# Performance work log

Measured on AMD Instinct MI355X. Metric: run time of the kernel, lower is better.

## Reference

```python
import jax, jax.numpy as jnp
import numpy as np
import math

B, M, N = 1, 128, 256
LIG_C = 256      # rep_1d num_c
ATTN_C = 32      # attention_num_c
HEADS = 8        # num_heads
EPS = 1e-5


def setup_inputs() -> dict:
    key = jax.random.key(0)
    ks = jax.random.split(key, 8)
    s = 1.0 / math.sqrt(LIG_C)
    return {
        "lig_profile": jax.random.normal(ks[0], (B, M, N, LIG_C), dtype=jnp.float32),
        "ln_scale": jnp.ones((LIG_C,), dtype=jnp.float32),
        "ln_bias": jnp.zeros((LIG_C,), dtype=jnp.float32),
        "wq": jax.random.normal(ks[1], (LIG_C, ATTN_C * HEADS), dtype=jnp.float32) * s,
        "wk": jax.random.normal(ks[2], (LIG_C, ATTN_C * HEADS), dtype=jnp.float32) * s,
        "wv": jax.random.normal(ks[3], (LIG_C, ATTN_C * HEADS), dtype=jnp.float32) * s,
        "wf": jax.random.normal(ks[4], (ATTN_C * HEADS, LIG_C), dtype=jnp.float32) * s,
        "bf": jnp.zeros((LIG_C,), dtype=jnp.float32),
    }


def reference(lig_profile, ln_scale, ln_bias, wq, wk, wv, wf, bf):
    # LayerNorm over channel dim
    mu = jnp.mean(lig_profile, axis=-1, keepdims=True)
    var = jnp.mean(jnp.square(lig_profile - mu), axis=-1, keepdims=True)
    x = (lig_profile - mu) * jax.lax.rsqrt(var + EPS) * ln_scale + ln_bias

    # QKV projections; view splits last dim as (attn_c, heads) -> channel-major layout
    shape5 = x.shape[:-1] + (ATTN_C, HEADS)
    q = (x @ wq).reshape(shape5)  # [b,m,n,c,h]
    k = (x @ wk).reshape(shape5)
    v = (x @ wv).reshape(shape5)

    factor = 1.0 / math.sqrt(ATTN_C)
    aff = jnp.einsum('bmich,bmjch->bmijh', q, k) * factor  # [b,m,i,j,h]
    weights = jax.nn.softmax(aff, axis=-2)                  # softmax over j (keys)
    out = jnp.einsum('bmrch,bmirh->bmich', v, weights)      # [b,m,i,c,h]
    out = out.reshape(out.shape[:-2] + (ATTN_C * HEADS,))
    return out @ wf + bf
```

## Files before the change

### kernel.cpp

```cpp
#include <hip/hip_runtime.h>

typedef _Float16 f16;
typedef _Float16 f16x8 __attribute__((ext_vector_type(8)));
typedef _Float16 f16x4 __attribute__((ext_vector_type(4)));
typedef float f32x4 __attribute__((ext_vector_type(4)));

#define MDIM 128
#define NDIM 256
#define CDIM 256
#define ROWS (MDIM*NDIM)

__global__ __launch_bounds__(256) void k_prep(
    const float* __restrict__ wq, const float* __restrict__ wk,
    const float* __restrict__ wv, const float* __restrict__ wf,
    f16* __restrict__ bq, f16* __restrict__ bk, f16* __restrict__ bv,
    f16* __restrict__ bw)
{
  int idx   = blockIdx.x & 255;
  int which = blockIdx.x >> 8;
  int kk    = threadIdx.x;
  if (which < 3) {
    const float* W = which == 0 ? wq : which == 1 ? wk : wv;
    f16* dst       = which == 0 ? bq : which == 1 ? bk : bv;
    float sc = which == 0 ? 0.17677669529663689f : 1.0f;
    int j = (idx & 31) * 8 + (idx >> 5);
    dst[idx * 256 + kk] = (f16)(W[(size_t)kk * 256 + j] * sc);
  } else {
    int pk = (kk & 31) * 8 + (kk >> 5);
    bw[idx * 256 + kk] = (f16)wf[(size_t)pk * 256 + idx];
  }
}

__global__ __launch_bounds__(256) void k_ln(const float* __restrict__ x,
                                            const float* __restrict__ g,
                                            const float* __restrict__ b,
                                            f16* __restrict__ y)
{
  int row  = blockIdx.x * 4 + (threadIdx.x >> 6);
  int lane = threadIdx.x & 63;
  const float4 xv = *(const float4*)(x + (size_t)row * CDIM + lane * 4);
  float s  = xv.x + xv.y + xv.z + xv.w;
  float s2 = xv.x*xv.x + xv.y*xv.y + xv.z*xv.z + xv.w*xv.w;
#pragma unroll
  for (int m = 1; m < 64; m <<= 1) {
    s  += __shfl_xor(s,  m, 64);
    s2 += __shfl_xor(s2, m, 64);
  }
  float mu  = s * (1.0f / CDIM);
  float var = s2 * (1.0f / CDIM) - mu * mu;
  float rs  = rsqrtf(var + 1e-5f);
  const float4 gv = *(const float4*)(g + lane * 4);
  const float4 bv = *(const float4*)(b + lane * 4);
  f16x4 o;
  o[0] = (f16)((xv.x - mu) * rs * gv.x + bv.x);
  o[1] = (f16)((xv.y - mu) * rs * gv.y + bv.y);
  o[2] = (f16)((xv.z - mu) * rs * gv.z + bv.z);
  o[3] = (f16)((xv.w - mu) * rs * gv.w + bv.w);
  *(f16x4*)(y + (size_t)row * CDIM + lane * 4) = o;
}

__global__ __launch_bounds__(256) void k_qkv(const f16* __restrict__ x,
    const f16* __restrict__ bq, const f16* __restrict__ bk, const f16* __restrict__ bv,
    f16* __restrict__ q, f16* __restrict__ k, f16* __restrict__ v)
{
  __shared__ f16 As[64][264];
  __shared__ f16 Bs[64][264];
  int bm = blockIdx.x;
  int t = threadIdx.x, lane = t & 63, w = t >> 6;
  int wr = w >> 1, wc = w & 1;
  int l15 = lane & 15, l4 = lane >> 4;
#pragma unroll
  for (int p = 0; p < 8; ++p) {
    int r = t >> 2, c0 = (t & 3) * 8 + p * 32;
    *(f16x8*)&As[r][c0] = *(const f16x8*)(x + (size_t)(bm * 64 + r) * 256 + c0);
  }
  for (int ct = 0; ct < 12; ++ct) {
    const f16* B = ct < 4 ? bq : ct < 8 ? bk : bv;
    f16* dst     = ct < 4 ? q  : ct < 8 ? k  : v;
    int je0 = (ct & 3) * 64;
#pragma unroll
    for (int p = 0; p < 8; ++p) {
      int r = t >> 2, c0 = (t & 3) * 8 + p * 32;
      *(f16x8*)&Bs[r][c0] = *(const f16x8*)(B + (size_t)(je0 + r) * 256 + c0);
    }
    __syncthreads();
    f32x4 acc[2][2] = {};
#pragma unroll
    for (int kt = 0; kt < 8; ++kt) {
      f16x8 a0 = *(const f16x8*)&As[wr * 32 +      l15][kt * 32 + l4 * 8];
      f16x8 a1 = *(const f16x8*)&As[wr * 32 + 16 + l15][kt * 32 + l4 * 8];
      f16x8 b0 = *(const f16x8*)&Bs[wc * 32 +      l15][kt * 32 + l4 * 8];
      f16x8 b1 = *(const f16x8*)&Bs[wc * 32 + 16 + l15][kt * 32 + l4 * 8];
      acc[0][0] = __builtin_amdgcn_mfma_f32_16x16x32_f16(a0, b0, acc[0][0], 0, 0, 0);
      acc[0][1] = __builtin_amdgcn_mfma_f32_16x16x32_f16(a0, b1, acc[0][1], 0, 0, 0);
      acc[1][0] = __builtin_amdgcn_mfma_f32_16x16x32_f16(a1, b0, acc[1][0], 0, 0, 0);
      acc[1][1] = __builtin_amdgcn_mfma_f32_16x16x32_f16(a1, b1, acc[1][1], 0, 0, 0);
    }
#pragma unroll
    for (int mi = 0; mi < 2; ++mi)
#pragma unroll
      for (int ni = 0; ni < 2; ++ni)
#pragma unroll
        for (int r = 0; r < 4; ++r) {
          int row = bm * 64 + wr * 32 + mi * 16 + l4 * 4 + r;
          int col = je0 + wc * 32 + ni * 16 + l15;
          dst[(size_t)row * 256 + col] = (f16)acc[mi][ni][r];
        }
    __syncthreads();
  }
}

__global__ __launch_bounds__(256) void k_attn(const f16* __restrict__ q,
    const f16* __restrict__ k, const f16* __restrict__ v, f16* __restrict__ o)
{
  __shared__ f16 ks[256][40];
  __shared__ f16 vt[32][264];
  __shared__ f16 ps[4][16][264];
  int m = blockIdx.x >> 3, h = blockIdx.x & 7;
  int t = threadIdx.x, lane = t & 63, w = t >> 6;
  int l15 = lane & 15, l4 = lane >> 4;
  size_t base = ((size_t)m * 256) * 256 + h * 32;
#pragma unroll
  for (int p = 0; p < 4; ++p) {
    int n = p * 64 + (t >> 2);
    int c0 = (t & 3) * 8;
    *(f16x8*)&ks[n][c0] = *(const f16x8*)(k + base + (size_t)n * 256 + c0);
    f16x8 vv = *(const f16x8*)(v + base + (size_t)n * 256 + c0);
#pragma unroll
    for (int i = 0; i < 8; ++i) vt[c0 + i][n] = vv[i];
  }
  __syncthreads();
  for (int ch = 0; ch < 4; ++ch) {
    int i0 = w * 64 + ch * 16;
    f16x8 qa = *(const f16x8*)(q + base + (size_t)(i0 + l15) * 256 + l4 * 8);
    f32x4 s[16];
#pragma unroll
    for (int jf = 0; jf < 16; ++jf) {
      f16x8 kb = *(const f16x8*)&ks[jf * 16 + l15][l4 * 8];
      f32x4 z = {0.f, 0.f, 0.f, 0.f};
      s[jf] = __builtin_amdgcn_mfma_f32_16x16x32_f16(qa, kb, z, 0, 0, 0);
    }
#pragma unroll
    for (int r = 0; r < 4; ++r) {
      float mx = s[0][r];
#pragma unroll
      for (int jf = 1; jf < 16; ++jf) mx = fmaxf(mx, s[jf][r]);
      mx = fmaxf(mx, __shfl_xor(mx, 1, 64));
      mx = fmaxf(mx, __shfl_xor(mx, 2, 64));
      mx = fmaxf(mx, __shfl_xor(mx, 4, 64));
      mx = fmaxf(mx, __shfl_xor(mx, 8, 64));
      float sum = 0.f;
#pragma unroll
      for (int jf = 0; jf < 16; ++jf) {
        float e = __expf(s[jf][r] - mx);
        s[jf][r] = e;
        sum += e;
      }
      sum += __shfl_xor(sum, 1, 64);
      sum += __shfl_xor(sum, 2, 64);
      sum += __shfl_xor(sum, 4, 64);
      sum += __shfl_xor(sum, 8, 64);
      float inv = 1.f / sum;
#pragma unroll
      for (int jf = 0; jf < 16; ++jf)
        ps[w][l4 * 4 + r][jf * 16 + l15] = (f16)(s[jf][r] * inv);
    }
    f32x4 o0 = {0.f,0.f,0.f,0.f}, o1 = {0.f,0.f,0.f,0.f};
#pragma unroll
    for (int kk = 0; kk < 8; ++kk) {
      f16x8 pa  = *(const f16x8*)&ps[w][l15][kk * 32 + l4 * 8];
      f16x8 vb0 = *(const f16x8*)&vt[l15][kk * 32 + l4 * 8];
      f16x8 vb1 = *(const f16x8*)&vt[16 + l15][kk * 32 + l4 * 8];
      o0 = __builtin_amdgcn_mfma_f32_16x16x32_f16(pa, vb0, o0, 0, 0, 0);
      o1 = __builtin_amdgcn_mfma_f32_16x16x32_f16(pa, vb1, o1, 0, 0, 0);
    }
#pragma unroll
    for (int r = 0; r < 4; ++r) {
      size_t ro = base + (size_t)(i0 + l4 * 4 + r) * 256;
      o[ro + l15]      = (f16)o0[r];
      o[ro + 16 + l15] = (f16)o1[r];
    }
  }
}

__global__ __launch_bounds__(256) void k_out(const f16* __restrict__ a,
    const f16* __restrict__ bw, const float* __restrict__ bias,
    float* __restrict__ out)
{
  __shared__ f16 As[64][264];
  __shared__ f16 Bs[64][264];
  int bm = blockIdx.x;
  int t = threadIdx.x, lane = t & 63, w = t >> 6;
  int wr = w >> 1, wc = w & 1;
  int l15 = lane & 15, l4 = lane >> 4;
#pragma unroll
  for (int p = 0; p < 8; ++p) {
    int r = t >> 2, c0 = (t & 3) * 8 + p * 32;
    *(f16x8*)&As[r][c0] = *(const f16x8*)(a + (size_t)(bm * 64 + r) * 256 + c0);
  }
  for (int ct = 0; ct < 4; ++ct) {
    int col0 = ct * 64;
#pragma unroll
    for (int p = 0; p < 8; ++p) {
      int r = t >> 2, c0 = (t & 3) * 8 + p * 32;
      *(f16x8*)&Bs[r][c0] = *(const f16x8*)(bw + (size_t)(col0 + r) * 256 + c0);
    }
    __syncthreads();
    f32x4 acc[2][2] = {};
#pragma unroll
    for (int kt = 0; kt < 8; ++kt) {
      f16x8 a0 = *(const f16x8*)&As[wr * 32 +      l15][kt * 32 + l4 * 8];
      f16x8 a1 = *(const f16x8*)&As[wr * 32 + 16 + l15][kt * 32 + l4 * 8];
      f16x8 b0 = *(const f16x8*)&Bs[wc * 32 +      l15][kt * 32 + l4 * 8];
      f16x8 b1 = *(const f16x8*)&Bs[wc * 32 + 16 + l15][kt * 32 + l4 * 8];
      acc[0][0] = __builtin_amdgcn_mfma_f32_16x16x32_f16(a0, b0, acc[0][0], 0, 0, 0);
      acc[0][1] = __builtin_amdgcn_mfma_f32_16x16x32_f16(a0, b1, acc[0][1], 0, 0, 0);
      acc[1][0] = __builtin_amdgcn_mfma_f32_16x16x32_f16(a1, b0, acc[1][0], 0, 0, 0);
      acc[1][1] = __builtin_amdgcn_mfma_f32_16x16x32_f16(a1, b1, acc[1][1], 0, 0, 0);
    }
#pragma unroll
    for (int mi = 0; mi < 2; ++mi)
#pragma unroll
      for (int ni = 0; ni < 2; ++ni)
#pragma unroll
        for (int r = 0; r < 4; ++r) {
          int row = bm * 64 + wr * 32 + mi * 16 + l4 * 4 + r;
          int col = col0 + wc * 32 + ni * 16 + l15;
          out[(size_t)row * 256 + col] = acc[mi][ni][r] + bias[col];
        }
    __syncthreads();
  }
}

extern "C" void kernel_launch(void* const* d_in, const int* in_sizes, int n_in,
                              void* d_out, int out_size, void* d_ws, size_t ws_size,
                              hipStream_t stream)
{
  const float* x  = (const float*)d_in[0];
  const float* g  = (const float*)d_in[1];
  const float* b  = (const float*)d_in[2];
  const float* wq = (const float*)d_in[3];
  const float* wk = (const float*)d_in[4];
  const float* wv = (const float*)d_in[5];
  const float* wf = (const float*)d_in[6];
  const float* bf = (const float*)d_in[7];
  float* out = (float*)d_out;

  char* ws = (char*)d_ws;
  f16* xh = (f16*)(ws);
  f16* qh = (f16*)(ws + (size_t)16 * 1024 * 1024);
  f16* kh = (f16*)(ws + (size_t)32 * 1024 * 1024);
  f16* vh = (f16*)(ws + (size_t)48 * 1024 * 1024);
  char* wbase = ws + (size_t)64 * 1024 * 1024;
  f16* bq = (f16*)(wbase);
  f16* bk = (f16*)(wbase + 128 * 1024);
  f16* bv = (f16*)(wbase + 256 * 1024);
  f16* bw = (f16*)(wbase + 384 * 1024);

  k_prep<<<1024,      256, 0, stream>>>(wq, wk, wv, wf, bq, bk, bv, bw);
  k_ln  <<<ROWS / 4,  256, 0, stream>>>(x, g, b, xh);
  k_qkv <<<ROWS / 64, 256, 0, stream>>>(xh, bq, bk, bv, qh, kh, vh);
  k_attn<<<MDIM * 8,  256, 0, stream>>>(qh, kh, vh, xh);
  k_out <<<ROWS / 64, 256, 0, stream>>>(xh, bw, bf, out);
}
```

Measured before the change: 98.34 us.

## Fuse LayerNorm into QKV GEMM, emit transposed V, use flash-style 32x32 attention

LayerNorm is fused into the QKV projection kernel, which removes one launch and the fp16 activation round trip through memory. The QKV kernel now writes V pre-transposed through an LDS staging tile, so the attention kernel loads it with vectorized reads instead of scalar transposed stores. Attention is rewritten as an online-softmax loop using 32x32x16 MFMAs, exp2 with log2(e) folded into the Q weights, and a lazy rescale that skips rescaling when the running max changes little. Probabilities are passed between lanes with shuffles instead of LDS, and the grid is split into query halves to give more blocks. The cost is more shuffle traffic and more complex register-level data movement.

Result: faster. 84.05 us (-14.5%).

```diff
diff --git a/kernel.cpp b/kernel.cpp
--- a/kernel.cpp
+++ b/kernel.cpp
@@ -3,12 +3,20 @@
 typedef _Float16 f16;
 typedef _Float16 f16x8 __attribute__((ext_vector_type(8)));
 typedef _Float16 f16x4 __attribute__((ext_vector_type(4)));
+typedef _Float16 f16x2 __attribute__((ext_vector_type(2)));
 typedef float f32x4 __attribute__((ext_vector_type(4)));
+typedef float f32x16 __attribute__((ext_vector_type(16)));
 
 #define MDIM 128
 #define NDIM 256
 #define CDIM 256
 #define ROWS (MDIM*NDIM)
+
+__device__ inline int pk2(float a, float b) {
+  union { f16x2 h; int i; } u;
+  u.h[0] = (f16)a; u.h[1] = (f16)b;
+  return u.i;
+}
 
 __global__ __launch_bounds__(256) void k_prep(
     const float* __restrict__ wq, const float* __restrict__ wk,
@@ -22,61 +30,52 @@
   if (which < 3) {
     const float* W = which == 0 ? wq : which == 1 ? wk : wv;
     f16* dst       = which == 0 ? bq : which == 1 ? bk : bv;
-    float sc = which == 0 ? 0.17677669529663689f : 1.0f;
+    float sc = which == 0 ? (0.17677669529663689f * 1.4426950408889634f) : 1.0f;
     int j = (idx & 31) * 8 + (idx >> 5);
     dst[idx * 256 + kk] = (f16)(W[(size_t)kk * 256 + j] * sc);
   } else {
-    int pk = (kk & 31) * 8 + (kk >> 5);
-    bw[idx * 256 + kk] = (f16)wf[(size_t)pk * 256 + idx];
-  }
-}
-
-__global__ __launch_bounds__(256) void k_ln(const float* __restrict__ x,
-                                            const float* __restrict__ g,
-                                            const float* __restrict__ b,
-                                            f16* __restrict__ y)
-{
-  int row  = blockIdx.x * 4 + (threadIdx.x >> 6);
-  int lane = threadIdx.x & 63;
-  const float4 xv = *(const float4*)(x + (size_t)row * CDIM + lane * 4);
-  float s  = xv.x + xv.y + xv.z + xv.w;
-  float s2 = xv.x*xv.x + xv.y*xv.y + xv.z*xv.z + xv.w*xv.w;
-#pragma unroll
-  for (int m = 1; m < 64; m <<= 1) {
-    s  += __shfl_xor(s,  m, 64);
-    s2 += __shfl_xor(s2, m, 64);
-  }
-  float mu  = s * (1.0f / CDIM);
-  float var = s2 * (1.0f / CDIM) - mu * mu;
-  float rs  = rsqrtf(var + 1e-5f);
-  const float4 gv = *(const float4*)(g + lane * 4);
-  const float4 bv = *(const float4*)(b + lane * 4);
-  f16x4 o;
-  o[0] = (f16)((xv.x - mu) * rs * gv.x + bv.x);
-  o[1] = (f16)((xv.y - mu) * rs * gv.y + bv.y);
-  o[2] = (f16)((xv.z - mu) * rs * gv.z + bv.z);
-  o[3] = (f16)((xv.w - mu) * rs * gv.w + bv.w);
-  *(f16x4*)(y + (size_t)row * CDIM + lane * 4) = o;
-}
-
-__global__ __launch_bounds__(256) void k_qkv(const f16* __restrict__ x,
+    int pkk = (kk & 31) * 8 + (kk >> 5);
+    bw[idx * 256 + kk] = (f16)wf[(size_t)pkk * 256 + idx];
+  }
+}
+
+__global__ __launch_bounds__(256) void k_lnqkv(const float* __restrict__ x,
+    const float* __restrict__ g, const float* __restrict__ bb,
     const f16* __restrict__ bq, const f16* __restrict__ bk, const f16* __restrict__ bv,
-    f16* __restrict__ q, f16* __restrict__ k, f16* __restrict__ v)
+    f16* __restrict__ qo, f16* __restrict__ ko, f16* __restrict__ vT)
 {
   __shared__ f16 As[64][264];
   __shared__ f16 Bs[64][264];
+  __shared__ f16 vtmp[64][72];
   int bm = blockIdx.x;
   int t = threadIdx.x, lane = t & 63, w = t >> 6;
   int wr = w >> 1, wc = w & 1;
   int l15 = lane & 15, l4 = lane >> 4;
-#pragma unroll
-  for (int p = 0; p < 8; ++p) {
-    int r = t >> 2, c0 = (t & 3) * 8 + p * 32;
-    *(f16x8*)&As[r][c0] = *(const f16x8*)(x + (size_t)(bm * 64 + r) * 256 + c0);
+  const float4 gv  = *(const float4*)(g + lane * 4);
+  const float4 bv4 = *(const float4*)(bb + lane * 4);
+#pragma unroll 4
+  for (int rr = 0; rr < 16; ++rr) {
+    int r = w * 16 + rr;
+    const float4 xv = *(const float4*)(x + (size_t)(bm * 64 + r) * 256 + lane * 4);
+    float s  = xv.x + xv.y + xv.z + xv.w;
+    float s2 = xv.x*xv.x + xv.y*xv.y + xv.z*xv.z + xv.w*xv.w;
+#pragma unroll
+    for (int mm = 1; mm < 64; mm <<= 1) {
+      s  += __shfl_xor(s,  mm, 64);
+      s2 += __shfl_xor(s2, mm, 64);
+    }
+    float mu  = s * (1.0f / 256.0f);
+    float var = s2 * (1.0f / 256.0f) - mu * mu;
+    float rs  = rsqrtf(var + 1e-5f);
+    f16x4 ov;
+    ov[0] = (f16)((xv.x - mu) * rs * gv.x + bv4.x);
+    ov[1] = (f16)((xv.y - mu) * rs * gv.y + bv4.y);
+    ov[2] = (f16)((xv.z - mu) * rs * gv.z + bv4.z);
+    ov[3] = (f16)((xv.w - mu) * rs * gv.w + bv4.w);
+    *(f16x4*)&As[r][lane * 4] = ov;
   }
   for (int ct = 0; ct < 12; ++ct) {
     const f16* B = ct < 4 ? bq : ct < 8 ? bk : bv;
-    f16* dst     = ct < 4 ? q  : ct < 8 ? k  : v;
     int je0 = (ct & 3) * 64;
 #pragma unroll
     for (int p = 0; p < 8; ++p) {
@@ -96,90 +95,123 @@
       acc[1][0] = __builtin_amdgcn_mfma_f32_16x16x32_f16(a1, b0, acc[1][0], 0, 0, 0);
       acc[1][1] = __builtin_amdgcn_mfma_f32_16x16x32_f16(a1, b1, acc[1][1], 0, 0, 0);
     }
-#pragma unroll
-    for (int mi = 0; mi < 2; ++mi)
-#pragma unroll
-      for (int ni = 0; ni < 2; ++ni)
-#pragma unroll
-        for (int r = 0; r < 4; ++r) {
-          int row = bm * 64 + wr * 32 + mi * 16 + l4 * 4 + r;
-          int col = je0 + wc * 32 + ni * 16 + l15;
-          dst[(size_t)row * 256 + col] = (f16)acc[mi][ni][r];
-        }
-    __syncthreads();
-  }
-}
-
-__global__ __launch_bounds__(256) void k_attn(const f16* __restrict__ q,
-    const f16* __restrict__ k, const f16* __restrict__ v, f16* __restrict__ o)
+    if (ct < 8) {
+      f16* dst = ct < 4 ? qo : ko;
+#pragma unroll
+      for (int mi = 0; mi < 2; ++mi)
+#pragma unroll
+        for (int ni = 0; ni < 2; ++ni)
+#pragma unroll
+          for (int r = 0; r < 4; ++r) {
+            int row = bm * 64 + wr * 32 + mi * 16 + l4 * 4 + r;
+            int col = je0 + wc * 32 + ni * 16 + l15;
+            dst[(size_t)row * 256 + col] = (f16)acc[mi][ni][r];
+          }
+    } else {
+#pragma unroll
+      for (int mi = 0; mi < 2; ++mi)
+#pragma unroll
+        for (int ni = 0; ni < 2; ++ni)
+#pragma unroll
+          for (int r = 0; r < 4; ++r)
+            vtmp[wc * 32 + ni * 16 + l15][wr * 32 + mi * 16 + l4 * 4 + r] = (f16)acc[mi][ni][r];
+      __syncthreads();
+      int ch = t >> 2, np = (t & 3) * 16;
+      size_t gdst = ((size_t)(bm >> 2) * 256 + je0 + ch) * 256 + (bm & 3) * 64 + np;
+      *(f16x8*)(vT + gdst)     = *(const f16x8*)&vtmp[ch][np];
+      *(f16x8*)(vT + gdst + 8) = *(const f16x8*)&vtmp[ch][np + 8];
+    }
+    __syncthreads();
+  }
+}
+
+__global__ __launch_bounds__(256, 4) void k_attn(const f16* __restrict__ q,
+    const f16* __restrict__ k, const f16* __restrict__ vT, f16* __restrict__ o)
 {
   __shared__ f16 ks[256][40];
   __shared__ f16 vt[32][264];
-  __shared__ f16 ps[4][16][264];
-  int m = blockIdx.x >> 3, h = blockIdx.x & 7;
+  int bx = blockIdx.x;
+  int m = bx >> 4, h = (bx >> 1) & 7, half = bx & 1;
   int t = threadIdx.x, lane = t & 63, w = t >> 6;
-  int l15 = lane & 15, l4 = lane >> 4;
-  size_t base = ((size_t)m * 256) * 256 + h * 32;
+  int i32 = lane & 31, hi = lane >> 5;
+  size_t rowbase = (size_t)m * 256;
 #pragma unroll
   for (int p = 0; p < 4; ++p) {
     int n = p * 64 + (t >> 2);
     int c0 = (t & 3) * 8;
-    *(f16x8*)&ks[n][c0] = *(const f16x8*)(k + base + (size_t)n * 256 + c0);
-    f16x8 vv = *(const f16x8*)(v + base + (size_t)n * 256 + c0);
-#pragma unroll
-    for (int i = 0; i < 8; ++i) vt[c0 + i][n] = vv[i];
+    *(f16x8*)&ks[n][c0] = *(const f16x8*)(k + (rowbase + n) * 256 + h * 32 + c0);
+  }
+#pragma unroll
+  for (int p = 0; p < 4; ++p) {
+    int idx = p * 256 + t;
+    int c = idx >> 5, nb = (idx & 31) * 8;
+    *(f16x8*)&vt[c][nb] = *(const f16x8*)(vT + ((size_t)m * 256 + h * 32 + c) * 256 + nb);
   }
   __syncthreads();
-  for (int ch = 0; ch < 4; ++ch) {
-    int i0 = w * 64 + ch * 16;
-    f16x8 qa = *(const f16x8*)(q + base + (size_t)(i0 + l15) * 256 + l4 * 8);
-    f32x4 s[16];
-#pragma unroll
-    for (int jf = 0; jf < 16; ++jf) {
-      f16x8 kb = *(const f16x8*)&ks[jf * 16 + l15][l4 * 8];
-      f32x4 z = {0.f, 0.f, 0.f, 0.f};
-      s[jf] = __builtin_amdgcn_mfma_f32_16x16x32_f16(qa, kb, z, 0, 0, 0);
-    }
-#pragma unroll
-    for (int r = 0; r < 4; ++r) {
-      float mx = s[0][r];
-#pragma unroll
-      for (int jf = 1; jf < 16; ++jf) mx = fmaxf(mx, s[jf][r]);
-      mx = fmaxf(mx, __shfl_xor(mx, 1, 64));
-      mx = fmaxf(mx, __shfl_xor(mx, 2, 64));
-      mx = fmaxf(mx, __shfl_xor(mx, 4, 64));
-      mx = fmaxf(mx, __shfl_xor(mx, 8, 64));
-      float sum = 0.f;
-#pragma unroll
-      for (int jf = 0; jf < 16; ++jf) {
-        float e = __expf(s[jf][r] - mx);
-        s[jf][r] = e;
-        sum += e;
-      }
-      sum += __shfl_xor(sum, 1, 64);
-      sum += __shfl_xor(sum, 2, 64);
-      sum += __shfl_xor(sum, 4, 64);
-      sum += __shfl_xor(sum, 8, 64);
-      float inv = 1.f / sum;
-#pragma unroll
-      for (int jf = 0; jf < 16; ++jf)
-        ps[w][l4 * 4 + r][jf * 16 + l15] = (f16)(s[jf][r] * inv);
-    }
-    f32x4 o0 = {0.f,0.f,0.f,0.f}, o1 = {0.f,0.f,0.f,0.f};
-#pragma unroll
-    for (int kk = 0; kk < 8; ++kk) {
-      f16x8 pa  = *(const f16x8*)&ps[w][l15][kk * 32 + l4 * 8];
-      f16x8 vb0 = *(const f16x8*)&vt[l15][kk * 32 + l4 * 8];
-      f16x8 vb1 = *(const f16x8*)&vt[16 + l15][kk * 32 + l4 * 8];
-      o0 = __builtin_amdgcn_mfma_f32_16x16x32_f16(pa, vb0, o0, 0, 0, 0);
-      o1 = __builtin_amdgcn_mfma_f32_16x16x32_f16(pa, vb1, o1, 0, 0, 0);
-    }
-#pragma unroll
-    for (int r = 0; r < 4; ++r) {
-      size_t ro = base + (size_t)(i0 + l4 * 4 + r) * 256;
-      o[ro + l15]      = (f16)o0[r];
-      o[ro + 16 + l15] = (f16)o1[r];
-    }
+  int qi0 = half * 128 + w * 32;
+  const f16* qp = q + (rowbase + qi0 + i32) * 256 + h * 32 + hi * 8;
+  f16x8 qf0 = *(const f16x8*)(qp);
+  f16x8 qf1 = *(const f16x8*)(qp + 16);
+  f32x16 O = {};
+  float m_run = -1e30f, l_run = 0.f;
+#pragma unroll 2
+  for (int kb = 0; kb < 8; ++kb) {
+    f16x8 kf0 = *(const f16x8*)&ks[kb * 32 + i32][hi * 8];
+    f16x8 kf1 = *(const f16x8*)&ks[kb * 32 + i32][16 + hi * 8];
+    f32x16 s = {};
+    s = __builtin_amdgcn_mfma_f32_32x32x16_f16(kf0, qf0, s, 0, 0, 0);
+    s = __builtin_amdgcn_mfma_f32_32x32x16_f16(kf1, qf1, s, 0, 0, 0);
+    float pmax = s[0];
+#pragma unroll
+    for (int r = 1; r < 16; ++r) pmax = fmaxf(pmax, s[r]);
+    pmax = fmaxf(pmax, __shfl_xor(pmax, 32, 64));
+    if (!__all(pmax - m_run <= 8.f)) {
+      float m_new = fmaxf(m_run, pmax);
+      float f = __builtin_amdgcn_exp2f(m_run - m_new);
+      l_run *= f;
+#pragma unroll
+      for (int r = 0; r < 16; ++r)
+        O[r] *= __shfl(f, (r & 3) + 8 * (r >> 2) + 4 * hi, 64);
+      m_run = m_new;
+    }
+    float lsum = 0.f;
+#pragma unroll
+    for (int r = 0; r < 16; ++r) {
+      float e = __builtin_amdgcn_exp2f(s[r] - m_run);
+      s[r] = e;
+      lsum += e;
+    }
+    lsum += __shfl_xor(lsum, 32, 64);
+    l_run += lsum;
+    int W0[4], W1[4];
+#pragma unroll
+    for (int qq = 0; qq < 4; ++qq) {
+      W0[qq] = pk2(s[4 * qq],     s[4 * qq + 1]);
+      W1[qq] = pk2(s[4 * qq + 2], s[4 * qq + 3]);
+    }
+#pragma unroll
+    for (int ks2 = 0; ks2 < 2; ++ks2) {
+      int X0 = W0[2 * ks2], Y0 = W0[2 * ks2 + 1];
+      int X1 = W1[2 * ks2], Y1 = W1[2 * ks2 + 1];
+      int a0 = __shfl(X0, i32, 64),      b0 = __shfl(Y0, i32, 64);
+      int a1 = __shfl(X1, i32, 64),      b1 = __shfl(Y1, i32, 64);
+      int a2 = __shfl(X0, i32 + 32, 64), b2 = __shfl(Y0, i32 + 32, 64);
+      int a3 = __shfl(X1, i32 + 32, 64), b3 = __shfl(Y1, i32 + 32, 64);
+      union { unsigned int ww[4]; f16x8 v; } pa;
+      pa.ww[0] = hi ? (unsigned)b0 : (unsigned)a0;
+      pa.ww[1] = hi ? (unsigned)b1 : (unsigned)a1;
+      pa.ww[2] = hi ? (unsigned)b2 : (unsigned)a2;
+      pa.ww[3] = hi ? (unsigned)b3 : (unsigned)a3;
+      f16x8 vb = *(const f16x8*)&vt[i32][kb * 32 + ks2 * 16 + hi * 8];
+      O = __builtin_amdgcn_mfma_f32_32x32x16_f16(pa.v, vb, O, 0, 0, 0);
+    }
+  }
+  float inv = 1.f / l_run;
+#pragma unroll
+  for (int r = 0; r < 16; ++r) {
+    int i = (r & 3) + 8 * (r >> 2) + 4 * hi;
+    float fr = __shfl(inv, i, 64);
+    o[(rowbase + (size_t)(qi0 + i)) * 256 + h * 32 + i32] = (f16)(O[r] * fr);
   }
 }
 
@@ -247,19 +279,18 @@
   float* out = (float*)d_out;
 
   char* ws = (char*)d_ws;
-  f16* xh = (f16*)(ws);
-  f16* qh = (f16*)(ws + (size_t)16 * 1024 * 1024);
-  f16* kh = (f16*)(ws + (size_t)32 * 1024 * 1024);
-  f16* vh = (f16*)(ws + (size_t)48 * 1024 * 1024);
+  f16* ah  = (f16*)(ws);
+  f16* qh  = (f16*)(ws + (size_t)16 * 1024 * 1024);
+  f16* kh  = (f16*)(ws + (size_t)32 * 1024 * 1024);
+  f16* vTh = (f16*)(ws + (size_t)48 * 1024 * 1024);
   char* wbase = ws + (size_t)64 * 1024 * 1024;
   f16* bq = (f16*)(wbase);
   f16* bk = (f16*)(wbase + 128 * 1024);
   f16* bv = (f16*)(wbase + 256 * 1024);
   f16* bw = (f16*)(wbase + 384 * 1024);
 
-  k_prep<<<1024,      256, 0, stream>>>(wq, wk, wv, wf, bq, bk, bv, bw);
-  k_ln  <<<ROWS / 4,  256, 0, stream>>>(x, g, b, xh);
-  k_qkv <<<ROWS / 64, 256, 0, stream>>>(xh, bq, bk, bv, qh, kh, vh);
-  k_attn<<<MDIM * 8,  256, 0, stream>>>(qh, kh, vh, xh);
-  k_out <<<ROWS / 64, 256, 0, stream>>>(xh, bw, bf, out);
-}
+  k_prep <<<1024, 256, 0, stream>>>(wq, wk, wv, wf, bq, bk, bv, bw);
+  k_lnqkv<<<512,  256, 0, stream>>>(x, g, b, bq, bk, bv, qh, kh, vTh);
+  k_attn <<<2048, 256, 0, stream>>>(qh, kh, vTh, ah);
+  k_out  <<<512,  256, 0, stream>>>(ah, bw, bf, out);
+}
```
